# Kernel optimization log

Measured on AMD Instinct MI355X. Metric: run time of the kernel, lower is better.

Reference implementation:

```python
import jax, jax.numpy as jnp
import numpy as np

EPS = 1e-5
KH = KW = 3  # deformable kernel
K = KH * KW


def _offset_conv(w, woff, boff):
    # standard 3x3 conv, stride 1, padding 1, NCHW
    out = jax.lax.conv_general_dilated(
        w, woff, window_strides=(1, 1), padding='SAME',
        dimension_numbers=('NCHW', 'OIHW', 'NCHW'))
    return out + boff[None, :, None, None]


def _deform_conv(feat, offset, wd, bd):
    # feat: [B,C,H,W]; offset: [B,2K,H,W] with (dy,dx) pairs per kernel point
    B, C, H, W = feat.shape
    off = offset.reshape(B, K, 2, H, W)
    ii = jnp.arange(H, dtype=feat.dtype)[:, None]  # [H,1]
    jj = jnp.arange(W, dtype=feat.dtype)[None, :]  # [1,W]
    kk = jnp.arange(K)
    ky = (kk // KW - 1).astype(feat.dtype)[None, :, None, None]  # [1,K,1,1]
    kx = (kk % KW - 1).astype(feat.dtype)[None, :, None, None]
    py = ii[None, None] + ky + off[:, :, 0]  # [B,K,H,W] sample rows
    px = jj[None, None] + kx + off[:, :, 1]  # [B,K,H,W] sample cols

    featf = feat.reshape(B, C, H * W)
    y0 = jnp.floor(py)
    x0 = jnp.floor(px)
    sampled = jnp.zeros((B, C, K, H, W), dtype=feat.dtype)
    for dy in (0, 1):
        for dx in (0, 1):
            yc = y0 + dy
            xc = x0 + dx
            wgt = (1.0 - jnp.abs(py - yc)) * (1.0 - jnp.abs(px - xc))
            valid = (yc >= 0) & (yc <= H - 1) & (xc >= 0) & (xc <= W - 1)
            wgt = jnp.where(valid, wgt, 0.0)  # zero padding outside
            yi = jnp.clip(yc, 0, H - 1).astype(jnp.int32)
            xi = jnp.clip(xc, 0, W - 1).astype(jnp.int32)
            idx = (yi * W + xi).reshape(B, 1, K * H * W)
            vals = jnp.take_along_axis(featf, idx, axis=2).reshape(B, C, K, H, W)
            sampled = sampled + vals * wgt[:, None]
    # weighted 3x3 conv over sampled points
    out = jnp.einsum('bckhw,ock->bohw', sampled, wd.reshape(wd.shape[0], C, K))
    return out + bd[None, :, None, None]


def setup_inputs() -> dict:
    key = jax.random.key(0)
    ks = jax.random.split(key, 13)
    B, Cin, H, W = 8, 256, 96, 96
    Cm = 64
    s1 = 1.0 / np.sqrt(Cin)
    s3 = 1.0 / np.sqrt(Cm * 9)
    return {
        'x': jax.random.normal(ks[0], (B, Cin, H, W), jnp.float32),
        'w1': jax.random.normal(ks[1], (Cm, Cin), jnp.float32) * s1,
        'b1': jax.random.normal(ks[2], (Cm,), jnp.float32) * s1,
        'woff': jax.random.normal(ks[3], (18, Cm, 3, 3), jnp.float32) * s3,
        'boff': jax.random.normal(ks[4], (18,), jnp.float32) * s3,
        'wd': jax.random.normal(ks[5], (Cm, Cm, 3, 3), jnp.float32) * s3,
        'bd': jax.random.normal(ks[6], (Cm,), jnp.float32) * s3,
        'gamma': jnp.ones((Cm,), jnp.float32),
        'beta': jnp.zeros((Cm,), jnp.float32),
        'rmean': jnp.zeros((Cm,), jnp.float32),
        'rvar': jax.random.uniform(ks[7], (Cm,), jnp.float32, 0.5, 1.5),
        'w2': jax.random.normal(ks[8], (Cin, Cm), jnp.float32) / np.sqrt(Cm),
        'b2': jax.random.normal(ks[9], (Cin,), jnp.float32) / np.sqrt(Cm),
    }


def reference(x, w1, b1, woff, boff, wd, bd, gamma, beta, rmean, rvar, w2, b2):
    # pwconv1 (1x1)
    w = jnp.einsum('bchw,oc->bohw', x, w1) + b1[None, :, None, None]
    # deformable 3x3 conv with predicted offsets
    off = _offset_conv(w, woff, boff)
    w = _deform_conv(w, off, wd, bd)
    # BatchNorm (eval mode, running stats)
    inv = gamma / jnp.sqrt(rvar + EPS)
    w = w * inv[None, :, None, None] + (beta - rmean * inv)[None, :, None, None]
    # pwconv2 (1x1) + sigmoid gate
    w = jnp.einsum('bchw,oc->bohw', w, w2) + b2[None, :, None, None]
    return x * jax.nn.sigmoid(w)
```

## Files before the change

kernel.cpp:

```cpp
#include <hip/hip_runtime.h>
#include <math.h>

#define H 96
#define W 96
#define HW 9216
#define B 8
#define CIN 256
#define CM 64
#define NPOS (B*HW)
#define NBLK (NPOS/64)

__device__ __forceinline__ int xswiz(int n) { return (n & 7) * 144 + (n >> 3); }

typedef float  f32x4  __attribute__((ext_vector_type(4)));
typedef short  bf16x8 __attribute__((ext_vector_type(8)));

#define OFF_WOFFT 0
#define OFF_BNS   10368
#define OFF_BNB   10432
#define OFF_WDB1  10496
#define OFF_WDB3  18688
#define OFF_WDB2  37120
#define OFF_FEAT  45312
#define OFF_FCL   4763904
#define OFF_OFFS  9482496
#define OFF_VCL   OFF_FEAT

__device__ __forceinline__ unsigned bfbits(float f) {
  union { float f; unsigned u; } c;
  c.f = f;
  return (c.u + 0x7FFFu + ((c.u >> 16) & 1u)) >> 16;
}
__device__ __forceinline__ short f2bf(float f) { return (short)bfbits(f); }
__device__ __forceinline__ unsigned pack2(float lo, float hi) {
  return bfbits(lo) | (bfbits(hi) << 16);
}

__device__ __forceinline__ bf16x8 cvt_frag(const float* p) {
  const float2* q = (const float2*)p;
  float2 a0 = q[0], a1 = q[1], a2 = q[2], a3 = q[3];
  union { unsigned u[4]; bf16x8 v; } r;
  r.u[0] = pack2(a0.x, a0.y);
  r.u[1] = pack2(a1.x, a1.y);
  r.u[2] = pack2(a2.x, a2.y);
  r.u[3] = pack2(a3.x, a3.y);
  return r.v;
}

__global__ __launch_bounds__(256) void k0_prep(
    const float* __restrict__ w1, const float* __restrict__ woff,
    const float* __restrict__ wd, const float* __restrict__ w2,
    const float* __restrict__ gamma, const float* __restrict__ beta,
    const float* __restrict__ rmean, const float* __restrict__ rvar,
    float* __restrict__ ws) {
  int i = blockIdx.x * 256 + threadIdx.x;
  if (i < 10368) {
    int c = i / 162, r = i - c * 162;
    int o = r / 9, k = r - o * 9;
    ws[OFF_WOFFT + i] = woff[(o * 64 + c) * 9 + k];
  } else if (i < 10432) {
    int o = i - 10368;
    float inv = gamma[o] / sqrtf(rvar[o] + 1e-5f);
    ws[OFF_BNS + o] = inv;
    ws[OFF_BNB + o] = beta[o] - rmean[o] * inv;
  } else if (i < 26816) {
    int j = i - 10432;
    int j8 = j & 7, lane = (j >> 3) & 63, nt = (j >> 9) & 3, kc = j >> 11;
    int n = nt * 16 + (lane & 15);
    int c = kc * 32 + ((lane >> 4) & 3) * 8 + j8;
    ((short*)(ws + OFF_WDB1))[j] = f2bf(w1[n * 256 + c]);
  } else if (i < 63680) {
    int j = i - 26816;
    int j8 = j & 7, lane = (j >> 3) & 63, nt = (j >> 9) & 3, kc = j >> 11;
    int n = nt * 16 + (lane & 15);
    int c = (kc & 1) * 32 + ((lane >> 4) & 3) * 8 + j8;
    int ks = kc >> 1;
    ((short*)(ws + OFF_WDB3))[j] = f2bf(wd[(n * 64 + c) * 9 + ks]);
  } else if (i < 80064) {
    int j = i - 63680;
    int j8 = j & 7, lane = (j >> 3) & 63, nt = (j >> 9) & 15, kc = j >> 13;
    int n = nt * 16 + (lane & 15);
    int c = kc * 32 + ((lane >> 4) & 3) * 8 + j8;
    ((short*)(ws + OFF_WDB2))[j] = f2bf(w2[n * 64 + c]);
  }
}

__global__ __launch_bounds__(256) void k1_pw1(
    const float* __restrict__ x, const short* __restrict__ wdb1,
    const float* __restrict__ b1, float* __restrict__ feat,
    float* __restrict__ fcl) {
  __shared__ float sA[64 * 66];
  int t = threadIdx.x;
  int lane = t & 63;
  int qq = __builtin_amdgcn_readfirstlane(t >> 6);
  int quad = lane >> 4, l15 = lane & 15;
  int mrow = qq * 16 + l15;
  int gpos0 = blockIdx.x * 64;
  int b = gpos0 / HW, hw0 = gpos0 - b * HW;
  f32x4 acc[4];
#pragma unroll
  for (int nt = 0; nt < 4; nt++) acc[nt] = (f32x4){0.f, 0.f, 0.f, 0.f};

  for (int c0 = 0; c0 < CIN; c0 += 64) {
#pragma unroll 4
    for (int it = 0; it < 16; it++) {
      int ci = it * 4 + quad;
      int p = qq * 16 + l15;
      sA[p * 66 + ci] = x[(size_t)(b * CIN + c0 + ci) * HW + hw0 + p];
    }
#pragma unroll
    for (int ch = 0; ch < 2; ch++) {
      bf16x8 af = cvt_frag(&sA[mrow * 66 + ch * 32 + quad * 8]);
      int kc = (c0 >> 5) + ch;
#pragma unroll
      for (int nt = 0; nt < 4; nt++) {
        bf16x8 bf = ((const bf16x8*)wdb1)[(kc * 4 + nt) * 64 + lane];
        acc[nt] = __builtin_amdgcn_mfma_f32_16x16x32_bf16(af, bf, acc[nt], 0, 0, 0);
      }
    }
  }
  __syncthreads();
#pragma unroll
  for (int nt = 0; nt < 4; nt++) {
    int o = nt * 16 + l15;
#pragma unroll
    for (int reg = 0; reg < 4; reg++) {
      int m = qq * 16 + quad * 4 + reg;
      sA[m * 66 + o] = acc[nt][reg] + b1[o];
    }
  }
  __syncthreads();
  for (int rr = t; rr < 4096; rr += 256) {
    int o1 = rr >> 6, p1 = rr & 63;
    feat[(size_t)(b * CM + o1) * HW + hw0 + p1] = sA[p1 * 66 + o1];
    int p2 = rr >> 6, o2 = rr & 63;
    fcl[(size_t)(gpos0 + p2) * 64 + o2] = sA[p2 * 66 + o2];
  }
}

__global__ __launch_bounds__(256) void k2_off(
    const float* __restrict__ feat, const float* __restrict__ wofft,
    const float* __restrict__ boff, float* __restrict__ offs) {
  __shared__ float part[4 * 18 * 64];
  int t = threadIdx.x;
  int pos = t & 63;
  int gg = __builtin_amdgcn_readfirstlane(t >> 6);
  int gpos0 = xswiz(blockIdx.x) * 64;
  int b = gpos0 / HW, hw0 = gpos0 - b * HW;
  int hw = hw0 + pos;
  int i = hw / W, j = hw - i * W;
  int idx9[9];
  float m9[9];
#pragma unroll
  for (int kh = 0; kh < 3; kh++)
#pragma unroll
    for (int kw = 0; kw < 3; kw++) {
      int yy = i + kh - 1, xx = j + kw - 1;
      bool ok = (yy >= 0) && (yy < H) && (xx >= 0) && (xx < W);
      idx9[kh * 3 + kw] = ok ? yy * W + xx : 0;
      m9[kh * 3 + kw] = ok ? 1.f : 0.f;
    }
  const float* fb = feat + (size_t)b * CM * HW;
  float acc[18];
#pragma unroll
  for (int o = 0; o < 18; o++) acc[o] = 0.f;
  for (int cc = 0; cc < 16; cc++) {
    int c = gg * 16 + cc;
    const float* fc = fb + c * HW;
    float v[9];
#pragma unroll
    for (int k = 0; k < 9; k++) v[k] = fc[idx9[k]] * m9[k];
    const float* wr = wofft + c * 162;
#pragma unroll
    for (int o = 0; o < 18; o++)
#pragma unroll
      for (int k = 0; k < 9; k++)
        acc[o] += v[k] * wr[o * 9 + k];
  }
#pragma unroll
  for (int o = 0; o < 18; o++) part[(gg * 18 + o) * 64 + pos] = acc[o];
  __syncthreads();
  for (int r = t; r < 18 * 64; r += 256) {
    int o = r >> 6, p = r & 63;
    float s = part[o * 64 + p] + part[(18 + o) * 64 + p] +
              part[(36 + o) * 64 + p] + part[(54 + o) * 64 + p] + boff[o];
    offs[(size_t)b * 18 * HW + o * HW + hw0 + p] = s;
  }
}

__global__ __launch_bounds__(256) void k3_deform(
    const float* __restrict__ fcl, const float* __restrict__ offs,
    const short* __restrict__ wdb3, const float* __restrict__ bd,
    const float* __restrict__ bns, const float* __restrict__ bnb,
    float* __restrict__ vcl) {
  __shared__ float sA[64 * 66];
  __shared__ int   ti[4][576];
  __shared__ float tw[4][576];
  int t = threadIdx.x;
  int lane = t & 63;
  int qq = __builtin_amdgcn_readfirstlane(t >> 6);
  int quad = lane >> 4, l15 = lane & 15;
  int mrow = qq * 16 + l15;
  int gpos0 = xswiz(blockIdx.x) * 64;
  int b = gpos0 / HW, hw0 = gpos0 - b * HW;
  int hw = hw0 + lane;
  int i = hw / W, j = hw - i * W;
  const float* ob = offs + (size_t)b * 18 * HW + hw;

  for (int k = qq; k < 9; k += 4) {
    float dy = ob[(2 * k + 0) * HW];
    float dx = ob[(2 * k + 1) * HW];
    float py = (float)(i + k / 3 - 1) + dy;
    float px = (float)(j + k % 3 - 1) + dx;
    float y0f = floorf(py), x0f = floorf(px);
    int y0 = (int)y0f, x0 = (int)x0f;
    float fy = py - y0f, fx = px - x0f;
    float w00 = (1.f - fy) * (1.f - fx), w01 = (1.f - fy) * fx;
    float w10 = fy * (1.f - fx), w11 = fy * fx;
    bool vy0 = (y0 >= 0) && (y0 < H), vy1 = (y0 + 1 >= 0) && (y0 + 1 < H);
    bool vx0 = (x0 >= 0) && (x0 < W), vx1 = (x0 + 1 >= 0) && (x0 + 1 < W);
    if (!(vy0 && vx0)) w00 = 0.f;
    if (!(vy0 && vx1)) w01 = 0.f;
    if (!(vy1 && vx0)) w10 = 0.f;
    if (!(vy1 && vx1)) w11 = 0.f;
    int yi0 = min(max(y0, 0), H - 1), yi1 = min(max(y0 + 1, 0), H - 1);
    int xi0 = min(max(x0, 0), W - 1), xi1 = min(max(x0 + 1, 0), W - 1);
    int e = k * 64 + lane;
    ti[0][e] = (yi0 * W + xi0) * 64;  tw[0][e] = w00;
    ti[1][e] = (yi0 * W + xi1) * 64;  tw[1][e] = w01;
    ti[2][e] = (yi1 * W + xi0) * 64;  tw[2][e] = w10;
    ti[3][e] = (yi1 * W + xi1) * 64;  tw[3][e] = w11;
  }
  __syncthreads();

  const float* fb = fcl + (size_t)b * HW * 64 + lane;
  f32x4 acc[4];
#pragma unroll
  for (int nt = 0; nt < 4; nt++) acc[nt] = (f32x4){0.f, 0.f, 0.f, 0.f};

  for (int ks = 0; ks < 9; ks++) {
#pragma unroll 4
    for (int pp = 0; pp < 16; pp++) {
      int p2 = qq * 16 + pp;
      int e = ks * 64 + p2;
      float s = tw[0][e] * fb[ti[0][e]] + tw[1][e] * fb[ti[1][e]] +
                tw[2][e] * fb[ti[2][e]] + tw[3][e] * fb[ti[3][e]];
      sA[p2 * 66 + lane] = s;
    }
#pragma unroll
    for (int ch = 0; ch < 2; ch++) {
      bf16x8 af = cvt_frag(&sA[mrow * 66 + ch * 32 + quad * 8]);
      int kc = ks * 2 + ch;
#pragma unroll
      for (int nt = 0; nt < 4; nt++) {
        bf16x8 bf = ((const bf16x8*)wdb3)[(kc * 4 + nt) * 64 + lane];
        acc[nt] = __builtin_amdgcn_mfma_f32_16x16x32_bf16(af, bf, acc[nt], 0, 0, 0);
      }
    }
  }
  __syncthreads();
#pragma unroll
  for (int nt = 0; nt < 4; nt++) {
    int o = nt * 16 + l15;
    float sc = bns[o], sb = bnb[o], bb = bd[o];
#pragma unroll
    for (int reg = 0; reg < 4; reg++) {
      int m = qq * 16 + quad * 4 + reg;
      sA[m * 66 + o] = (acc[nt][reg] + bb) * sc + sb;
    }
  }
  __syncthreads();
  for (int rr = t; rr < 4096; rr += 256) {
    int p = rr >> 6, o = rr & 63;
    vcl[(size_t)(gpos0 + p) * 64 + o] = sA[p * 66 + o];
  }
}

__global__ __launch_bounds__(256) void k4_pw2(
    const float* __restrict__ x, const float* __restrict__ vcl,
    const short* __restrict__ wdb2, const float* __restrict__ b2,
    float* __restrict__ out) {
  __shared__ float sA[64 * 66];
  int t = threadIdx.x;
  int lane = t & 63;
  int qq = __builtin_amdgcn_readfirstlane(t >> 6);
  int quad = lane >> 4, l15 = lane & 15;
  int mrow = qq * 16 + l15;
  int gpos0 = blockIdx.x * 64;
  int b = gpos0 / HW, hw0 = gpos0 - b * HW;

#pragma unroll 4
  for (int it = 0; it < 16; it++) {
    int p = qq * 16 + it;
    sA[p * 66 + lane] = vcl[(size_t)(gpos0 + p) * 64 + lane];
  }
  bf16x8 af0 = cvt_frag(&sA[mrow * 66 + 0 * 32 + quad * 8]);
  bf16x8 af1 = cvt_frag(&sA[mrow * 66 + 1 * 32 + quad * 8]);

  f32x4 acc[16];
#pragma unroll
  for (int nt = 0; nt < 16; nt++) acc[nt] = (f32x4){0.f, 0.f, 0.f, 0.f};
#pragma unroll
  for (int nt = 0; nt < 16; nt++) {
    bf16x8 bf0 = ((const bf16x8*)wdb2)[(0 * 16 + nt) * 64 + lane];
    bf16x8 bf1 = ((const bf16x8*)wdb2)[(1 * 16 + nt) * 64 + lane];
    acc[nt] = __builtin_amdgcn_mfma_f32_16x16x32_bf16(af0, bf0, acc[nt], 0, 0, 0);
    acc[nt] = __builtin_amdgcn_mfma_f32_16x16x32_bf16(af1, bf1, acc[nt], 0, 0, 0);
  }
  for (int nc = 0; nc < 4; nc++) {
    __syncthreads();
#pragma unroll
    for (int nt2 = 0; nt2 < 4; nt2++) {
      int nt = nc * 4 + nt2;
      int o1 = nt2 * 16 + l15;
#pragma unroll
      for (int reg = 0; reg < 4; reg++) {
        int m = qq * 16 + quad * 4 + reg;
        sA[m * 66 + o1] = acc[nt][reg] + b2[nc * 64 + nt2 * 16 + l15];
      }
    }
    __syncthreads();
    for (int rr = t; rr < 4096; rr += 256) {
      int o1 = rr >> 6, p = rr & 63;
      int o = nc * 64 + o1;
      float wv = sA[p * 66 + o1];
      float sg = 1.f / (1.f + __expf(-wv));
      size_t gi = ((size_t)b * CIN + o) * HW + hw0 + p;
      out[gi] = x[gi] * sg;
    }
  }
}

extern "C" void kernel_launch(void* const* d_in, const int* in_sizes, int n_in,
                              void* d_out, int out_size, void* d_ws, size_t ws_size,
                              hipStream_t stream) {
  const float* x     = (const float*)d_in[0];
  const float* w1    = (const float*)d_in[1];
  const float* b1    = (const float*)d_in[2];
  const float* woff  = (const float*)d_in[3];
  const float* boff  = (const float*)d_in[4];
  const float* wd    = (const float*)d_in[5];
  const float* bd    = (const float*)d_in[6];
  const float* gamma = (const float*)d_in[7];
  const float* beta  = (const float*)d_in[8];
  const float* rmean = (const float*)d_in[9];
  const float* rvar  = (const float*)d_in[10];
  const float* w2    = (const float*)d_in[11];
  const float* b2    = (const float*)d_in[12];
  float* out = (float*)d_out;
  float* ws  = (float*)d_ws;

  dim3 blk(256);
  k0_prep<<<dim3(313), blk, 0, stream>>>(w1, woff, wd, w2, gamma, beta, rmean, rvar, ws);
  k1_pw1<<<dim3(NBLK), blk, 0, stream>>>(x, (const short*)(ws + OFF_WDB1), b1,
                                         ws + OFF_FEAT, ws + OFF_FCL);
  k2_off<<<dim3(NBLK), blk, 0, stream>>>(ws + OFF_FEAT, ws + OFF_WOFFT, boff, ws + OFF_OFFS);
  k3_deform<<<dim3(NBLK), blk, 0, stream>>>(ws + OFF_FCL, ws + OFF_OFFS,
                                            (const short*)(ws + OFF_WDB3), bd,
                                            ws + OFF_BNS, ws + OFF_BNB, ws + OFF_VCL);
  k4_pw2<<<dim3(NBLK), blk, 0, stream>>>(x, ws + OFF_VCL, (const short*)(ws + OFF_WDB2),
                                         b2, out);
}
```

Baseline: 297.4 us.

## Store deform output as bf16 and vectorize bilinear gathers with packed index/weight tables

The deform kernel now packs each bilinear corner's index and weight into one int2 LDS entry. Each lane gathers two adjacent channels with float2 loads, covering two positions per iteration. Sampled values are converted to bf16 once when written to shared memory, so the MFMA fragment is read directly without per-use conversion. The intermediate output passed to the pw2 kernel is stored as bf16 and loaded straight into MFMA fragments, halving that traffic and removing an LDS staging pass, at the cost of rounding the BN output to bf16 before storage (it was previously rounded only when loaded into the MFMA).

Result: no change. 302.6 us (+1.8%).

```diff
diff --git a/kernel.cpp b/kernel.cpp
--- a/kernel.cpp
+++ b/kernel.cpp
@@ -192,10 +192,9 @@
     const float* __restrict__ fcl, const float* __restrict__ offs,
     const short* __restrict__ wdb3, const float* __restrict__ bd,
     const float* __restrict__ bns, const float* __restrict__ bnb,
-    float* __restrict__ vcl) {
-  __shared__ float sA[64 * 66];
-  __shared__ int   ti[4][576];
-  __shared__ float tw[4][576];
+    short* __restrict__ vclb) {
+  __shared__ __align__(16) short sAb[64 * 72];
+  __shared__ int2 tiw[4][576];
   int t = threadIdx.x;
   int lane = t & 63;
   int qq = __builtin_amdgcn_readfirstlane(t >> 6);
@@ -226,30 +225,41 @@
     int yi0 = min(max(y0, 0), H - 1), yi1 = min(max(y0 + 1, 0), H - 1);
     int xi0 = min(max(x0, 0), W - 1), xi1 = min(max(x0 + 1, 0), W - 1);
     int e = k * 64 + lane;
-    ti[0][e] = (yi0 * W + xi0) * 64;  tw[0][e] = w00;
-    ti[1][e] = (yi0 * W + xi1) * 64;  tw[1][e] = w01;
-    ti[2][e] = (yi1 * W + xi0) * 64;  tw[2][e] = w10;
-    ti[3][e] = (yi1 * W + xi1) * 64;  tw[3][e] = w11;
-  }
-  __syncthreads();
-
-  const float* fb = fcl + (size_t)b * HW * 64 + lane;
+    tiw[0][e] = make_int2((yi0 * W + xi0) * 256, __float_as_int(w00));
+    tiw[1][e] = make_int2((yi0 * W + xi1) * 256, __float_as_int(w01));
+    tiw[2][e] = make_int2((yi1 * W + xi0) * 256, __float_as_int(w10));
+    tiw[3][e] = make_int2((yi1 * W + xi1) * 256, __float_as_int(w11));
+  }
+  __syncthreads();
+
+  const char* fbase = (const char*)fcl + (size_t)b * HW * 256;
+  int c2 = lane & 31;
+  int c28 = c2 * 8;
+  int half = lane >> 5;
+
   f32x4 acc[4];
 #pragma unroll
   for (int nt = 0; nt < 4; nt++) acc[nt] = (f32x4){0.f, 0.f, 0.f, 0.f};
 
   for (int ks = 0; ks < 9; ks++) {
 #pragma unroll 4
-    for (int pp = 0; pp < 16; pp++) {
-      int p2 = qq * 16 + pp;
-      int e = ks * 64 + p2;
-      float s = tw[0][e] * fb[ti[0][e]] + tw[1][e] * fb[ti[1][e]] +
-                tw[2][e] * fb[ti[2][e]] + tw[3][e] * fb[ti[3][e]];
-      sA[p2 * 66 + lane] = s;
+    for (int pp = 0; pp < 8; pp++) {
+      int pa = qq * 16 + pp * 2 + half;
+      int e = ks * 64 + pa;
+      int2 t0 = tiw[0][e], t1 = tiw[1][e], t2 = tiw[2][e], t3 = tiw[3][e];
+      float2 v0 = *(const float2*)(fbase + (t0.x + c28));
+      float2 v1 = *(const float2*)(fbase + (t1.x + c28));
+      float2 v2 = *(const float2*)(fbase + (t2.x + c28));
+      float2 v3 = *(const float2*)(fbase + (t3.x + c28));
+      float w0 = __int_as_float(t0.y), w1 = __int_as_float(t1.y);
+      float w2 = __int_as_float(t2.y), w3 = __int_as_float(t3.y);
+      float slo = w0 * v0.x + w1 * v1.x + w2 * v2.x + w3 * v3.x;
+      float shi = w0 * v0.y + w1 * v1.y + w2 * v2.y + w3 * v3.y;
+      ((unsigned*)sAb)[pa * 36 + c2] = pack2(slo, shi);
     }
 #pragma unroll
     for (int ch = 0; ch < 2; ch++) {
-      bf16x8 af = cvt_frag(&sA[mrow * 66 + ch * 32 + quad * 8]);
+      bf16x8 af = *(const bf16x8*)(sAb + mrow * 72 + ch * 32 + quad * 8);
       int kc = ks * 2 + ch;
 #pragma unroll
       for (int nt = 0; nt < 4; nt++) {
@@ -266,18 +276,18 @@
 #pragma unroll
     for (int reg = 0; reg < 4; reg++) {
       int m = qq * 16 + quad * 4 + reg;
-      sA[m * 66 + o] = (acc[nt][reg] + bb) * sc + sb;
-    }
-  }
-  __syncthreads();
-  for (int rr = t; rr < 4096; rr += 256) {
-    int p = rr >> 6, o = rr & 63;
-    vcl[(size_t)(gpos0 + p) * 64 + o] = sA[p * 66 + o];
+      sAb[m * 72 + o] = f2bf((acc[nt][reg] + bb) * sc + sb);
+    }
+  }
+  __syncthreads();
+  for (int rr = t; rr < 2048; rr += 256) {
+    int p = rr >> 5, cc = rr & 31;
+    ((unsigned*)vclb)[(size_t)(gpos0 + p) * 32 + cc] = ((unsigned*)sAb)[p * 36 + cc];
   }
 }
 
 __global__ __launch_bounds__(256) void k4_pw2(
-    const float* __restrict__ x, const float* __restrict__ vcl,
+    const float* __restrict__ x, const short* __restrict__ vclb,
     const short* __restrict__ wdb2, const float* __restrict__ b2,
     float* __restrict__ out) {
   __shared__ float sA[64 * 66];
@@ -289,13 +299,9 @@
   int gpos0 = blockIdx.x * 64;
   int b = gpos0 / HW, hw0 = gpos0 - b * HW;
 
-#pragma unroll 4
-  for (int it = 0; it < 16; it++) {
-    int p = qq * 16 + it;
-    sA[p * 66 + lane] = vcl[(size_t)(gpos0 + p) * 64 + lane];
-  }
-  bf16x8 af0 = cvt_frag(&sA[mrow * 66 + 0 * 32 + quad * 8]);
-  bf16x8 af1 = cvt_frag(&sA[mrow * 66 + 1 * 32 + quad * 8]);
+  const bf16x8* ap = (const bf16x8*)(vclb + (size_t)(gpos0 + mrow) * 64);
+  bf16x8 af0 = ap[quad];
+  bf16x8 af1 = ap[4 + quad];
 
   f32x4 acc[16];
 #pragma unroll
@@ -357,7 +363,8 @@
   k2_off<<<dim3(NBLK), blk, 0, stream>>>(ws + OFF_FEAT, ws + OFF_WOFFT, boff, ws + OFF_OFFS);
   k3_deform<<<dim3(NBLK), blk, 0, stream>>>(ws + OFF_FCL, ws + OFF_OFFS,
                                             (const short*)(ws + OFF_WDB3), bd,
-                                            ws + OFF_BNS, ws + OFF_BNB, ws + OFF_VCL);
-  k4_pw2<<<dim3(NBLK), blk, 0, stream>>>(x, ws + OFF_VCL, (const short*)(ws + OFF_WDB2),
-                                         b2, out);
-}
+                                            ws + OFF_BNS, ws + OFF_BNB,
+                                            (short*)(ws + OFF_VCL));
+  k4_pw2<<<dim3(NBLK), blk, 0, stream>>>(x, (const short*)(ws + OFF_VCL),
+                                         (const short*)(ws + OFF_WDB2), b2, out);
+}
```
